# Kernel tuning notes

Hardware: AMD Instinct MI355X
Metric: run time of the kernel (lower is better)

The kernel has to match this reference:

```python
import jax, jax.numpy as jnp
import numpy as np

EMBED_DIM = 512
NUM_HEADS = 16
WINDOW = 8
SHIFT = 4
NUM_PATCHES = 64
NEG_INF = -1e9


def _attention_mask():
    # group map over the full patch grid, as in calculate_attention_mask
    P, s, ws = NUM_PATCHES, SHIFT, WINDOW
    g = np.zeros((P, P), dtype=np.float32)
    g[:, -s:] = 1
    g[-s:, :] = 2
    g[-s:, -s:] = 3
    nw = P // ws
    # (h ws a, w ws b) -> (h*w, ws*ws)
    gw = g.reshape(nw, ws, nw, ws).transpose(0, 2, 1, 3).reshape(nw * nw, ws * ws)
    same = gw[:, None, :] == gw[:, :, None]  # column - row == 0 -> allowed
    return jnp.asarray(same)  # (nW, S, S) bool, True = keep


def setup_inputs() -> dict:
    key = jax.random.key(0)
    ks = jax.random.split(key, 5)
    B, P, C = 16, NUM_PATCHES, EMBED_DIM
    sd = 1.0 / np.sqrt(C)
    return {
        "x": jax.random.normal(ks[0], (B, P, P, C), dtype=jnp.float32),
        "w_qkv": jax.random.normal(ks[1], (3 * C, C), dtype=jnp.float32) * sd,
        "b_qkv": jax.random.normal(ks[2], (3 * C,), dtype=jnp.float32) * 0.02,
        "w_out": jax.random.normal(ks[3], (C, C), dtype=jnp.float32) * sd,
        "b_out": jax.random.normal(ks[4], (C,), dtype=jnp.float32) * 0.02,
    }


def reference(x, w_qkv, b_qkv, w_out, b_out):
    B, P, _, C = x.shape
    ws, H = WINDOW, NUM_HEADS
    d = C // H
    nw = P // ws
    S = ws * ws
    scale = d ** (-0.5)

    # shift (roll backwards)
    xs = jnp.roll(x, (-SHIFT, -SHIFT), axis=(1, 2))
    # window partition: (B, nw, ws, nw, ws, C) -> (B*nw*nw, S, C)
    xw = xs.reshape(B, nw, ws, nw, ws, C).transpose(0, 1, 3, 2, 4, 5)
    xw = xw.reshape(B * nw * nw, S, C)

    qkv = xw @ w_qkv.T + b_qkv  # (Bn, S, 3C)
    q, k, v = jnp.split(qkv, 3, axis=-1)
    # head partition: (Bn, S, H, d) -> (Bn, H, S, d)
    part = lambda t: t.reshape(-1, S, H, d).transpose(0, 2, 1, 3)
    q, k, v = part(q), part(k), part(v)

    scores = jnp.einsum('bhqd,bhkd->bhqk', q, k) * scale  # (Bn, H, S, S)

    mask = _attention_mask()  # (nW, S, S) bool
    scores = scores.reshape(B, nw * nw, H, S, S)
    scores = jnp.where(mask[None, :, None], scores, NEG_INF)
    attn = jax.nn.softmax(scores, axis=-1)  # dropout p=0 (inference)
    attn = attn.reshape(B * nw * nw, H, S, S)

    out = jnp.einsum('bhqk,bhkd->bhqd', attn, v)  # (Bn, H, S, d)
    out = out.transpose(0, 2, 1, 3).reshape(B * nw * nw, S, C)  # merge heads
    out = out @ w_out.T + b_out

    # window merge: (B*nw*nw, S, C) -> (B, P, P, C)
    out = out.reshape(B, nw, nw, ws, ws, C).transpose(0, 1, 3, 2, 4, 5)
    out = out.reshape(B, P, P, C)
    # roll forwards
    return jnp.roll(out, (SHIFT, SHIFT), axis=(1, 2))
```

## Files before the change

### kernel.cpp

```cpp
#include <hip/hip_runtime.h>


using f16   = _Float16;
using f16x8 = __attribute__((ext_vector_type(8))) _Float16;
using f16x4 = __attribute__((ext_vector_type(4))) _Float16;
using f32x4 = __attribute__((ext_vector_type(4))) float;

#define MFMA16(a, b, c) __builtin_amdgcn_mfma_f32_16x16x32_f16((a), (b), (c), 0, 0, 0)
#define SCHEDBAR() __builtin_amdgcn_sched_barrier(0)
#define VMCNT0() asm volatile("s_waitcnt vmcnt(0)" ::: "memory")
#define LGKM0()  asm volatile("s_waitcnt lgkmcnt(0)" ::: "memory")
#define BAR()    __builtin_amdgcn_s_barrier()

static constexpr int QK_HALF = 65536 * 512;

__device__ __forceinline__ void nts4f(f32x4 v, float* p) {
  __builtin_nontemporal_store(v, (f32x4*)p);
}

__device__ __forceinline__ int tok2patch(int t) {
  int b = t >> 12, rem = t & 4095;
  int widx = rem >> 6, s = rem & 63;
  int pr = (((widx >> 3) << 3) + (s >> 3) + 4) & 63;
  int pc = (((widx & 7) << 3) + (s & 7) + 4) & 63;
  return ((b << 12) | (pr << 6) | pc) << 9;
}

__device__ __forceinline__ f16x8 cvt8(float4 a, float4 b) {
  f16x8 h = { (f16)a.x, (f16)a.y, (f16)a.z, (f16)a.w,
              (f16)b.x, (f16)b.y, (f16)b.z, (f16)b.w };
  return h;
}

__global__ __launch_bounds__(512, 2) void k_qkv(const float* __restrict__ x,
                                                const float* __restrict__ wq,
                                                const float* __restrict__ bq,
                                                f16* __restrict__ qk,
                                                f16* __restrict__ vt) {
  __shared__ __align__(16) char smem[86016];
  f16* const B0 = (f16*)smem;
  f16* const B1 = (f16*)(smem + 8192);

  const int tid = threadIdx.x;
  const int lane = tid & 63, wave = tid >> 6;
  const int jlo = lane & 15, g = lane >> 4;
  const int bm = blockIdx.x;

  const int nl = tid >> 2, kq = tid & 3;
  const int bslot = (kq ^ ((nl >> 1) & 3)) * 8;

  const int r0 = tok2patch(bm * 256 + wave * 32 + jlo);
  const int r1 = tok2patch(bm * 256 + wave * 32 + 16 + jlo);
  f16x8 af[2][16];
#pragma unroll
  for (int kg = 0; kg < 4; ++kg) {
    float4 t0[4][2], t1[4][2];
#pragma unroll
    for (int k4 = 0; k4 < 4; ++k4) {
      const int ko = (kg * 4 + k4) * 32 + g * 8;
      t0[k4][0] = *(const float4*)(x + r0 + ko);
      t0[k4][1] = *(const float4*)(x + r0 + ko + 4);
      t1[k4][0] = *(const float4*)(x + r1 + ko);
      t1[k4][1] = *(const float4*)(x + r1 + ko + 4);
    }
#pragma unroll
    for (int k4 = 0; k4 < 4; ++k4) {
      af[0][kg * 4 + k4] = cvt8(t0[k4][0], t0[k4][1]);
      af[1][kg * 4 + k4] = cvt8(t1[k4][0], t1[k4][1]);
    }
    SCHEDBAR();
  }

  f32x4 acc[2][8] = {};
  float4 rb[2];
#define LOADB(U2)                                                         \
  do {                                                                    \
    const int bn2_ = (U2) >> 4, k2_ = ((U2) & 15) * 32;                   \
    const float* bs_ = wq + (bn2_ * 128 + nl) * 512 + k2_ + kq * 8;       \
    rb[0] = *(const float4*)(bs_); rb[1] = *(const float4*)(bs_ + 4);     \
  } while (0)
#define WRITEB(Bp) do { *(f16x8*)((Bp) + nl * 32 + bslot) = cvt8(rb[0], rb[1]); } while (0)

  LOADB(0);
  SCHEDBAR();
  VMCNT0();
  WRITEB(B0);
  LOADB(1);
  LGKM0();
  BAR();

#pragma unroll 1
  for (int bn = 0; bn < 12; ++bn) {
    f16* const Cw = (f16*)(smem + 16384 + wave * 8704);
#pragma unroll
    for (int ks = 0; ks < 16; ++ks) {
      const int u = bn * 16 + ks;
      f16* const Bc = (u & 1) ? B1 : B0;
      f16* const Bn = (u & 1) ? B0 : B1;
      f16x8 bf[8];
#pragma unroll
      for (int nt = 0; nt < 8; ++nt) {
        const int n = nt * 16 + jlo;
        bf[nt] = *(const f16x8*)(Bc + n * 32 + ((g ^ ((n >> 1) & 3)) * 8));
      }
      __builtin_amdgcn_s_setprio(1);
#pragma unroll
      for (int mt = 0; mt < 2; ++mt)
#pragma unroll
        for (int nt = 0; nt < 8; ++nt)
          acc[mt][nt] = MFMA16(af[mt][ks], bf[nt], acc[mt][nt]);
      __builtin_amdgcn_s_setprio(0);
      VMCNT0();
      if (u + 1 < 192) WRITEB(Bn);
      SCHEDBAR();
      if (u + 2 < 192) LOADB(u + 2);
      LGKM0();
      BAR();
    }
    float bias[8];
#pragma unroll
    for (int nt = 0; nt < 8; ++nt) bias[nt] = bq[bn * 128 + nt * 16 + jlo];
    if (bn < 8) {
#pragma unroll
      for (int mt = 0; mt < 2; ++mt)
#pragma unroll
        for (int nt = 0; nt < 8; ++nt)
#pragma unroll
          for (int r = 0; r < 4; ++r)
            Cw[(mt * 16 + g * 4 + r) * 136 + nt * 16 + jlo] =
                (f16)(acc[mt][nt][r] + bias[nt]);
      LGKM0();
      f16* const gb = (bn < 4) ? (qk + bn * 128) : (qk + QK_HALF + (bn - 4) * 128);
#pragma unroll
      for (int p = 0; p < 8; ++p) {
        const int lr = (p >> 1) * 8 + (lane >> 3);
        const int ch = (p & 1) * 8 + (lane & 7);
        const int trow = bm * 256 + wave * 32 + lr;
        *(f16x8*)(gb + trow * 512 + ch * 8) = *(const f16x8*)(Cw + lr * 136 + ch * 8);
      }
    } else {
      const int w = (bm * 256 + wave * 32) >> 6;
      const int s0 = (wave * 32) & 63;
#pragma unroll
      for (int hf = 0; hf < 2; ++hf) {
#pragma unroll
        for (int n2 = 0; n2 < 4; ++n2) {
          const int nt = hf * 4 + n2;
#pragma unroll
          for (int mt = 0; mt < 2; ++mt) {
            f16x4 pk = { (f16)(acc[mt][nt][0] + bias[nt]), (f16)(acc[mt][nt][1] + bias[nt]),
                         (f16)(acc[mt][nt][2] + bias[nt]), (f16)(acc[mt][nt][3] + bias[nt]) };
            *(f16x4*)(Cw + (n2 * 16 + jlo) * 48 + mt * 16 + g * 4) = pk;
          }
        }
        LGKM0();
#pragma unroll
        for (int p = 0; p < 4; ++p) {
          const int cl = p * 16 + (lane >> 2);
          const int ch = lane & 3;
          const int n = (bn - 8) * 128 + hf * 64 + cl;
          const int h = n >> 5, d = n & 31;
          *(f16x8*)(vt + ((w * 16 + h) * 32 + d) * 64 + s0 + ch * 8) =
              *(const f16x8*)(Cw + cl * 48 + ch * 8);
        }
      }
    }
#pragma unroll
    for (int mt = 0; mt < 2; ++mt)
#pragma unroll
      for (int nt = 0; nt < 8; ++nt)
        acc[mt][nt] = (f32x4){0.f, 0.f, 0.f, 0.f};
  }
#undef LOADB
#undef WRITEB
}

__global__ __launch_bounds__(256) void k_attn(const f16* __restrict__ qk,
                                              const f16* __restrict__ vt,
                                              f16* __restrict__ ao) {
  __shared__ f16 P[4][64 * 72];
  const int w = blockIdx.x;
  const int widx = w & 63;
  const bool er = (widx >> 3) == 7;
  const bool ec = (widx & 7) == 7;
  const int tid = threadIdx.x;
  const int lane = tid & 63, wave = tid >> 6;
  const int jlo = lane & 15, g = lane >> 4;
  const int tb = w * 64;
  f16* Pw = P[wave];
  const float scale = 0.17677669529663687f;

#pragma unroll 1
  for (int hh = 0; hh < 4; ++hh) {
    const int h = wave * 4 + hh;
    f16x8 qa[4], kb[4];
#pragma unroll
    for (int mt = 0; mt < 4; ++mt)
      qa[mt] = *(const f16x8*)(qk + (tb + mt * 16 + jlo) * 512 + h * 32 + g * 8);
#pragma unroll
    for (int nt = 0; nt < 4; ++nt)
      kb[nt] = *(const f16x8*)(qk + QK_HALF + (tb + nt * 16 + jlo) * 512 + h * 32 + g * 8);
    f32x4 sc[4][4] = {};
#pragma unroll
    for (int mt = 0; mt < 4; ++mt)
#pragma unroll
      for (int nt = 0; nt < 4; ++nt)
        sc[mt][nt] = MFMA16(qa[mt], kb[nt], sc[mt][nt]);

    int gj[4];
#pragma unroll
    for (int nt = 0; nt < 4; ++nt) {
      int j = nt * 16 + jlo;
      gj[nt] = ((er && ((j >> 3) >= 4)) ? 2 : 0) | ((ec && ((j & 7) >= 4)) ? 1 : 0);
    }
    float rinv[4][4];
#pragma unroll
    for (int mt = 0; mt < 4; ++mt) {
#pragma unroll
      for (int r = 0; r < 4; ++r) {
        const int i = mt * 16 + g * 4 + r;
        const int gi = ((er && ((i >> 3) >= 4)) ? 2 : 0) | ((ec && ((i & 7) >= 4)) ? 1 : 0);
        float v0 = (gi == gj[0]) ? sc[mt][0][r] * scale : -1e9f;
        float v1 = (gi == gj[1]) ? sc[mt][1][r] * scale : -1e9f;
        float v2 = (gi == gj[2]) ? sc[mt][2][r] * scale : -1e9f;
        float v3 = (gi == gj[3]) ? sc[mt][3][r] * scale : -1e9f;
        float m = fmaxf(fmaxf(v0, v1), fmaxf(v2, v3));
        m = fmaxf(m, __shfl_xor(m, 1));
        m = fmaxf(m, __shfl_xor(m, 2));
        m = fmaxf(m, __shfl_xor(m, 4));
        m = fmaxf(m, __shfl_xor(m, 8));
        float p0 = __expf(v0 - m), p1 = __expf(v1 - m);
        float p2 = __expf(v2 - m), p3 = __expf(v3 - m);
        float s = p0 + p1 + p2 + p3;
        s += __shfl_xor(s, 1);
        s += __shfl_xor(s, 2);
        s += __shfl_xor(s, 4);
        s += __shfl_xor(s, 8);
        rinv[mt][r] = 1.0f / s;
        sc[mt][0][r] = p0; sc[mt][1][r] = p1; sc[mt][2][r] = p2; sc[mt][3][r] = p3;
      }
    }
#pragma unroll
    for (int mt = 0; mt < 4; ++mt)
#pragma unroll
      for (int nt = 0; nt < 4; ++nt)
#pragma unroll
        for (int r = 0; r < 4; ++r)
          Pw[(mt * 16 + g * 4 + r) * 72 + nt * 16 + jlo] = (f16)sc[mt][nt][r];
    asm volatile("s_waitcnt lgkmcnt(0)" ::: "memory");

    f32x4 o[4][2] = {};
#pragma unroll
    for (int ks = 0; ks < 2; ++ks) {
      f16x8 pa[4], vb[2];
#pragma unroll
      for (int mt = 0; mt < 4; ++mt)
        pa[mt] = *(const f16x8*)((const char*)Pw + (mt * 16 + jlo) * 144 + ks * 64 + g * 16);
#pragma unroll
      for (int nt = 0; nt < 2; ++nt)
        vb[nt] = *(const f16x8*)(vt + ((w * 16 + h) * 32 + nt * 16 + jlo) * 64 + ks * 32 + g * 8);
#pragma unroll
      for (int mt = 0; mt < 4; ++mt)
#pragma unroll
        for (int nt = 0; nt < 2; ++nt)
          o[mt][nt] = MFMA16(pa[mt], vb[nt], o[mt][nt]);
    }
#pragma unroll
    for (int mt = 0; mt < 4; ++mt)
#pragma unroll
      for (int nt = 0; nt < 2; ++nt)
#pragma unroll
        for (int r = 0; r < 4; ++r)
          Pw[(mt * 16 + g * 4 + r) * 40 + nt * 16 + jlo] =
              (f16)(o[mt][nt][r] * rinv[mt][r]);
    f16* arow = ao + (tb + lane) * 512 + h * 32;
#pragma unroll
    for (int c = 0; c < 4; ++c)
      *(f16x8*)(arow + c * 8) = *(const f16x8*)(Pw + lane * 40 + c * 8);
  }
}

__global__ __launch_bounds__(512, 2) void k_out(const f16* __restrict__ ao,
                                                const float* __restrict__ wo,
                                                const float* __restrict__ bo,
                                                float* __restrict__ out) {
  __shared__ __align__(16) char smem[86016];
  f16* const B0 = (f16*)smem;
  f16* const B1 = (f16*)(smem + 8192);

  const int tid = threadIdx.x;
  const int lane = tid & 63, wave = tid >> 6;
  const int jlo = lane & 15, g = lane >> 4;
  const int bm = blockIdx.x;

  const int nl = tid >> 2, kq = tid & 3;
  const int bslot = (kq ^ ((nl >> 1) & 3)) * 8;

  const f16* const a0 = ao + (bm * 256 + wave * 32 + jlo) * 512 + g * 8;
  const f16* const a1 = a0 + 16 * 512;
  f16x8 af[2][16];
#pragma unroll
  for (int ks = 0; ks < 16; ++ks) {
    af[0][ks] = *(const f16x8*)(a0 + ks * 32);
    af[1][ks] = *(const f16x8*)(a1 + ks * 32);
  }

  f32x4 acc[2][8] = {};
  float4 rb[2];
#define LOADB(U2)                                                         \
  do {                                                                    \
    const int bn2_ = (U2) >> 4, k2_ = ((U2) & 15) * 32;                   \
    const float* bs_ = wo + (bn2_ * 128 + nl) * 512 + k2_ + kq * 8;       \
    rb[0] = *(const float4*)(bs_); rb[1] = *(const float4*)(bs_ + 4);     \
  } while (0)
#define WRITEB(Bp) do { *(f16x8*)((Bp) + nl * 32 + bslot) = cvt8(rb[0], rb[1]); } while (0)

  LOADB(0);
  SCHEDBAR();
  VMCNT0();
  WRITEB(B0);
  LOADB(1);
  LGKM0();
  BAR();

#pragma unroll 1
  for (int bn = 0; bn < 4; ++bn) {
    float* const Cw = (float*)(smem + 16384 + wave * 8704);
#pragma unroll
    for (int ks = 0; ks < 16; ++ks) {
      const int u = bn * 16 + ks;
      f16* const Bc = (u & 1) ? B1 : B0;
      f16* const Bn = (u & 1) ? B0 : B1;
      f16x8 bf[8];
#pragma unroll
      for (int nt = 0; nt < 8; ++nt) {
        const int n = nt * 16 + jlo;
        bf[nt] = *(const f16x8*)(Bc + n * 32 + ((g ^ ((n >> 1) & 3)) * 8));
      }
      __builtin_amdgcn_s_setprio(1);
#pragma unroll
      for (int mt = 0; mt < 2; ++mt)
#pragma unroll
        for (int nt = 0; nt < 8; ++nt)
          acc[mt][nt] = MFMA16(af[mt][ks], bf[nt], acc[mt][nt]);
      __builtin_amdgcn_s_setprio(0);
      VMCNT0();
      if (u + 1 < 64) WRITEB(Bn);
      SCHEDBAR();
      if (u + 2 < 64) LOADB(u + 2);
      LGKM0();
      BAR();
    }
#pragma unroll
    for (int hf = 0; hf < 2; ++hf) {
#pragma unroll
      for (int n2 = 0; n2 < 4; ++n2) {
        const int nt = hf * 4 + n2;
        const float bias = bo[bn * 128 + nt * 16 + jlo];
#pragma unroll
        for (int mt = 0; mt < 2; ++mt)
#pragma unroll
          for (int r = 0; r < 4; ++r)
            Cw[(mt * 16 + g * 4 + r) * 68 + n2 * 16 + jlo] = acc[mt][nt][r] + bias;
      }
      LGKM0();
#pragma unroll
      for (int p = 0; p < 8; ++p) {
        const int lr = (p >> 1) * 8 + (lane >> 3);
        const int ch = (p & 1) * 8 + (lane & 7);
        const int trow = bm * 256 + wave * 32 + lr;
        nts4f(*(const f32x4*)(Cw + lr * 68 + ch * 4),
              out + tok2patch(trow) + bn * 128 + hf * 64 + ch * 4);
      }
      LGKM0();
    }
#pragma unroll
    for (int mt = 0; mt < 2; ++mt)
#pragma unroll
      for (int nt = 0; nt < 8; ++nt)
        acc[mt][nt] = (f32x4){0.f, 0.f, 0.f, 0.f};
  }
#undef LOADB
#undef WRITEB
}

extern "C" void kernel_launch(void* const* d_in, const int* in_sizes, int n_in,
                              void* d_out, int out_size, void* d_ws, size_t ws_size,
                              hipStream_t stream) {
  const float* x  = (const float*)d_in[0];
  const float* wq = (const float*)d_in[1];
  const float* bq = (const float*)d_in[2];
  const float* wo = (const float*)d_in[3];
  const float* bo = (const float*)d_in[4];
  float* out = (float*)d_out;

  f16* qk = (f16*)d_out;
  f16* ao = (f16*)d_ws;
  f16* vt = (f16*)((char*)d_ws + (64u << 20));

  k_qkv<<<dim3(256), 512, 0, stream>>>(x, wq, bq, qk, vt);
  k_attn<<<dim3(1024), 256, 0, stream>>>(qk, vt, ao);
  k_out<<<dim3(256), 512, 0, stream>>>(ao, wo, bo, out);
}
```

Baseline: 377.4 us.

## Halve GEMM block size and deepen weight prefetch to two stages

Both projection GEMM kernels drop from 512-thread blocks covering 256 tokens to 256-thread blocks covering 128 tokens, and launch twice as many blocks. Each thread now loads 16 weight floats per stage. The prefetch is triple-buffered in registers and waits on vmcnt(4) instead of vmcnt(0), so global weight loads overlap with more MFMA work. The QKV epilogue is also split into two halves, which shrinks its LDS staging. The gain should come from more blocks over the CUs and hidden load latency, but each block now re-reads the weight matrix for only half as many tokens, doubling total weight traffic.

```diff
diff --git a/kernel.cpp b/kernel.cpp
--- a/kernel.cpp
+++ b/kernel.cpp
@@ -8,6 +8,7 @@
 
 #define MFMA16(a, b, c) __builtin_amdgcn_mfma_f32_16x16x32_f16((a), (b), (c), 0, 0, 0)
 #define SCHEDBAR() __builtin_amdgcn_sched_barrier(0)
+#define VMCNT4() asm volatile("s_waitcnt vmcnt(4)" ::: "memory")
 #define VMCNT0() asm volatile("s_waitcnt vmcnt(0)" ::: "memory")
 #define LGKM0()  asm volatile("s_waitcnt lgkmcnt(0)" ::: "memory")
 #define BAR()    __builtin_amdgcn_s_barrier()
@@ -32,12 +33,12 @@
   return h;
 }
 
-__global__ __launch_bounds__(512, 2) void k_qkv(const float* __restrict__ x,
+__global__ __launch_bounds__(256, 2) void k_qkv(const float* __restrict__ x,
                                                 const float* __restrict__ wq,
                                                 const float* __restrict__ bq,
                                                 f16* __restrict__ qk,
                                                 f16* __restrict__ vt) {
-  __shared__ __align__(16) char smem[86016];
+  __shared__ __align__(16) char smem[37376];
   f16* const B0 = (f16*)smem;
   f16* const B1 = (f16*)(smem + 8192);
 
@@ -46,11 +47,11 @@
   const int jlo = lane & 15, g = lane >> 4;
   const int bm = blockIdx.x;
 
-  const int nl = tid >> 2, kq = tid & 3;
-  const int bslot = (kq ^ ((nl >> 1) & 3)) * 8;
-
-  const int r0 = tok2patch(bm * 256 + wave * 32 + jlo);
-  const int r1 = tok2patch(bm * 256 + wave * 32 + 16 + jlo);
+  const int nl = tid >> 1, kh = (tid & 1) * 16;
+  const int bsw = (nl >> 1) & 3, bc0 = (tid & 1) * 2;
+
+  const int r0 = tok2patch(bm * 128 + wave * 32 + jlo);
+  const int r1 = tok2patch(bm * 128 + wave * 32 + 16 + jlo);
   f16x8 af[2][16];
 #pragma unroll
   for (int kg = 0; kg < 4; ++kg) {
@@ -72,26 +73,32 @@
   }
 
   f32x4 acc[2][8] = {};
-  float4 rb[2];
-#define LOADB(U2)                                                         \
+  float4 rbA[4], rbB[4];
+#define LOADB(U2, RB)                                                     \
   do {                                                                    \
     const int bn2_ = (U2) >> 4, k2_ = ((U2) & 15) * 32;                   \
-    const float* bs_ = wq + (bn2_ * 128 + nl) * 512 + k2_ + kq * 8;       \
-    rb[0] = *(const float4*)(bs_); rb[1] = *(const float4*)(bs_ + 4);     \
+    const float* bs_ = wq + (bn2_ * 128 + nl) * 512 + k2_ + kh;           \
+    RB[0] = *(const float4*)(bs_);     RB[1] = *(const float4*)(bs_ + 4); \
+    RB[2] = *(const float4*)(bs_ + 8); RB[3] = *(const float4*)(bs_ + 12);\
   } while (0)
-#define WRITEB(Bp) do { *(f16x8*)((Bp) + nl * 32 + bslot) = cvt8(rb[0], rb[1]); } while (0)
-
-  LOADB(0);
+#define WRITEB(Bp, RB)                                                       \
+  do {                                                                       \
+    *(f16x8*)((Bp) + nl * 32 + ((bc0 ^ bsw) * 8))       = cvt8(RB[0], RB[1]);\
+    *(f16x8*)((Bp) + nl * 32 + (((bc0 + 1) ^ bsw) * 8)) = cvt8(RB[2], RB[3]);\
+  } while (0)
+
+  LOADB(0, rbA);
   SCHEDBAR();
   VMCNT0();
-  WRITEB(B0);
-  LOADB(1);
+  WRITEB(B0, rbA);
+  LOADB(1, rbB);
+  LOADB(2, rbA);
   LGKM0();
   BAR();
 
 #pragma unroll 1
   for (int bn = 0; bn < 12; ++bn) {
-    f16* const Cw = (f16*)(smem + 16384 + wave * 8704);
+    f16* const Cw = (f16*)(smem + 16384) + wave * 2560;
 #pragma unroll
     for (int ks = 0; ks < 16; ++ks) {
       const int u = bn * 16 + ks;
@@ -110,10 +117,18 @@
         for (int nt = 0; nt < 8; ++nt)
           acc[mt][nt] = MFMA16(af[mt][ks], bf[nt], acc[mt][nt]);
       __builtin_amdgcn_s_setprio(0);
-      VMCNT0();
-      if (u + 1 < 192) WRITEB(Bn);
-      SCHEDBAR();
-      if (u + 2 < 192) LOADB(u + 2);
+      if (u + 1 < 192) {
+        if (u < 190) { VMCNT4(); } else { VMCNT0(); }
+        if ((ks & 1) == 0) {
+          WRITEB(Bn, rbB);
+          SCHEDBAR();
+          if (u + 3 < 192) LOADB(u + 3, rbB);
+        } else {
+          WRITEB(Bn, rbA);
+          SCHEDBAR();
+          if (u + 3 < 192) LOADB(u + 3, rbA);
+        }
+      }
       LGKM0();
       BAR();
     }
@@ -121,26 +136,33 @@
 #pragma unroll
     for (int nt = 0; nt < 8; ++nt) bias[nt] = bq[bn * 128 + nt * 16 + jlo];
     if (bn < 8) {
-#pragma unroll
-      for (int mt = 0; mt < 2; ++mt)
-#pragma unroll
-        for (int nt = 0; nt < 8; ++nt)
-#pragma unroll
-          for (int r = 0; r < 4; ++r)
-            Cw[(mt * 16 + g * 4 + r) * 136 + nt * 16 + jlo] =
-                (f16)(acc[mt][nt][r] + bias[nt]);
-      LGKM0();
       f16* const gb = (bn < 4) ? (qk + bn * 128) : (qk + QK_HALF + (bn - 4) * 128);
 #pragma unroll
-      for (int p = 0; p < 8; ++p) {
-        const int lr = (p >> 1) * 8 + (lane >> 3);
-        const int ch = (p & 1) * 8 + (lane & 7);
-        const int trow = bm * 256 + wave * 32 + lr;
-        *(f16x8*)(gb + trow * 512 + ch * 8) = *(const f16x8*)(Cw + lr * 136 + ch * 8);
+      for (int hf = 0; hf < 2; ++hf) {
+#pragma unroll
+        for (int n2 = 0; n2 < 4; ++n2) {
+          const int nt = hf * 4 + n2;
+#pragma unroll
+          for (int mt = 0; mt < 2; ++mt)
+#pragma unroll
+            for (int r = 0; r < 4; ++r)
+              Cw[(mt * 16 + g * 4 + r) * 72 + n2 * 16 + jlo] =
+                  (f16)(acc[mt][nt][r] + bias[nt]);
+        }
+        LGKM0();
+#pragma unroll
+        for (int p = 0; p < 4; ++p) {
+          const int lr = p * 8 + (lane >> 3);
+          const int ch = lane & 7;
+          const int trow = bm * 128 + wave * 32 + lr;
+          *(f16x8*)(gb + trow * 512 + hf * 64 + ch * 8) =
+              *(const f16x8*)(Cw + lr * 72 + ch * 8);
+        }
+        LGKM0();
       }
     } else {
-      const int w = (bm * 256 + wave * 32) >> 6;
-      const int s0 = (wave * 32) & 63;
+      const int w = bm * 2 + (wave >> 1);
+      const int s0 = (wave & 1) * 32;
 #pragma unroll
       for (int hf = 0; hf < 2; ++hf) {
 #pragma unroll
@@ -150,7 +172,7 @@
           for (int mt = 0; mt < 2; ++mt) {
             f16x4 pk = { (f16)(acc[mt][nt][0] + bias[nt]), (f16)(acc[mt][nt][1] + bias[nt]),
                          (f16)(acc[mt][nt][2] + bias[nt]), (f16)(acc[mt][nt][3] + bias[nt]) };
-            *(f16x4*)(Cw + (n2 * 16 + jlo) * 48 + mt * 16 + g * 4) = pk;
+            *(f16x4*)(Cw + (n2 * 16 + jlo) * 40 + mt * 16 + g * 4) = pk;
           }
         }
         LGKM0();
@@ -161,8 +183,9 @@
           const int n = (bn - 8) * 128 + hf * 64 + cl;
           const int h = n >> 5, d = n & 31;
           *(f16x8*)(vt + ((w * 16 + h) * 32 + d) * 64 + s0 + ch * 8) =
-              *(const f16x8*)(Cw + cl * 48 + ch * 8);
-        }
+              *(const f16x8*)(Cw + cl * 40 + ch * 8);
+        }
+        LGKM0();
       }
     }
 #pragma unroll
@@ -280,11 +303,11 @@
   }
 }
 
-__global__ __launch_bounds__(512, 2) void k_out(const f16* __restrict__ ao,
+__global__ __launch_bounds__(256, 2) void k_out(const f16* __restrict__ ao,
                                                 const float* __restrict__ wo,
                                                 const float* __restrict__ bo,
                                                 float* __restrict__ out) {
-  __shared__ __align__(16) char smem[86016];
+  __shared__ __align__(16) char smem[51200];
   f16* const B0 = (f16*)smem;
   f16* const B1 = (f16*)(smem + 8192);
 
@@ -293,10 +316,10 @@
   const int jlo = lane & 15, g = lane >> 4;
   const int bm = blockIdx.x;
 
-  const int nl = tid >> 2, kq = tid & 3;
-  const int bslot = (kq ^ ((nl >> 1) & 3)) * 8;
-
-  const f16* const a0 = ao + (bm * 256 + wave * 32 + jlo) * 512 + g * 8;
+  const int nl = tid >> 1, kh = (tid & 1) * 16;
+  const int bsw = (nl >> 1) & 3, bc0 = (tid & 1) * 2;
+
+  const f16* const a0 = ao + (bm * 128 + wave * 32 + jlo) * 512 + g * 8;
   const f16* const a1 = a0 + 16 * 512;
   f16x8 af[2][16];
 #pragma unroll
@@ -306,26 +329,32 @@
   }
 
   f32x4 acc[2][8] = {};
-  float4 rb[2];
-#define LOADB(U2)                                                         \
+  float4 rbA[4], rbB[4];
+#define LOADB(U2, RB)                                                     \
   do {                                                                    \
     const int bn2_ = (U2) >> 4, k2_ = ((U2) & 15) * 32;                   \
-    const float* bs_ = wo + (bn2_ * 128 + nl) * 512 + k2_ + kq * 8;       \
-    rb[0] = *(const float4*)(bs_); rb[1] = *(const float4*)(bs_ + 4);     \
+    const float* bs_ = wo + (bn2_ * 128 + nl) * 512 + k2_ + kh;           \
+    RB[0] = *(const float4*)(bs_);     RB[1] = *(const float4*)(bs_ + 4); \
+    RB[2] = *(const float4*)(bs_ + 8); RB[3] = *(const float4*)(bs_ + 12);\
   } while (0)
-#define WRITEB(Bp) do { *(f16x8*)((Bp) + nl * 32 + bslot) = cvt8(rb[0], rb[1]); } while (0)
-
-  LOADB(0);
+#define WRITEB(Bp, RB)                                                       \
+  do {                                                                       \
+    *(f16x8*)((Bp) + nl * 32 + ((bc0 ^ bsw) * 8))       = cvt8(RB[0], RB[1]);\
+    *(f16x8*)((Bp) + nl * 32 + (((bc0 + 1) ^ bsw) * 8)) = cvt8(RB[2], RB[3]);\
+  } while (0)
+
+  LOADB(0, rbA);
   SCHEDBAR();
   VMCNT0();
-  WRITEB(B0);
-  LOADB(1);
+  WRITEB(B0, rbA);
+  LOADB(1, rbB);
+  LOADB(2, rbA);
   LGKM0();
   BAR();
 
 #pragma unroll 1
   for (int bn = 0; bn < 4; ++bn) {
-    float* const Cw = (float*)(smem + 16384 + wave * 8704);
+    float* const Cw = (float*)((char*)smem + 16384) + wave * 2176;
 #pragma unroll
     for (int ks = 0; ks < 16; ++ks) {
       const int u = bn * 16 + ks;
@@ -344,10 +373,18 @@
         for (int nt = 0; nt < 8; ++nt)
           acc[mt][nt] = MFMA16(af[mt][ks], bf[nt], acc[mt][nt]);
       __builtin_amdgcn_s_setprio(0);
-      VMCNT0();
-      if (u + 1 < 64) WRITEB(Bn);
-      SCHEDBAR();
-      if (u + 2 < 64) LOADB(u + 2);
+      if (u + 1 < 64) {
+        if (u < 62) { VMCNT4(); } else { VMCNT0(); }
+        if ((ks & 1) == 0) {
+          WRITEB(Bn, rbB);
+          SCHEDBAR();
+          if (u + 3 < 64) LOADB(u + 3, rbB);
+        } else {
+          WRITEB(Bn, rbA);
+          SCHEDBAR();
+          if (u + 3 < 64) LOADB(u + 3, rbA);
+        }
+      }
       LGKM0();
       BAR();
     }
@@ -368,7 +405,7 @@
       for (int p = 0; p < 8; ++p) {
         const int lr = (p >> 1) * 8 + (lane >> 3);
         const int ch = (p & 1) * 8 + (lane & 7);
-        const int trow = bm * 256 + wave * 32 + lr;
+        const int trow = bm * 128 + wave * 32 + lr;
         nts4f(*(const f32x4*)(Cw + lr * 68 + ch * 4),
               out + tok2patch(trow) + bn * 128 + hf * 64 + ch * 4);
       }
@@ -398,7 +435,7 @@
   f16* ao = (f16*)d_ws;
   f16* vt = (f16*)((char*)d_ws + (64u << 20));
 
-  k_qkv<<<dim3(256), 512, 0, stream>>>(x, wq, bq, qk, vt);
+  k_qkv<<<dim3(512), 256, 0, stream>>>(x, wq, bq, qk, vt);
   k_attn<<<dim3(1024), 256, 0, stream>>>(qk, vt, ao);
-  k_out<<<dim3(256), 512, 0, stream>>>(ao, wo, bo, out);
-}
+  k_out<<<dim3(512), 256, 0, stream>>>(ao, wo, bo, out);
+}
```

New measurement: 417.6 us. 10.6% more time.

## Pre-convert weights to fp16 and stream them via direct global-to-LDS loads

Applied to the files above, without the earlier changes.

Adds a small kernel that converts the QKV and output projection weights to fp16 in a pre-swizzled layout once per call. The GEMM kernels then stage 64-wide K slices straight into LDS with global_load_lds instead of loading fp32 to registers, converting, and writing to LDS. This halves the per-step barrier count and the weight bytes read by every block. The cost is an extra launch plus a larger LDS footprint, with __syncthreads replacing the manual waitcnt pipelining.

```diff
diff --git a/kernel.cpp b/kernel.cpp
--- a/kernel.cpp
+++ b/kernel.cpp
@@ -8,11 +8,18 @@
 
 #define MFMA16(a, b, c) __builtin_amdgcn_mfma_f32_16x16x32_f16((a), (b), (c), 0, 0, 0)
 #define SCHEDBAR() __builtin_amdgcn_sched_barrier(0)
-#define VMCNT0() asm volatile("s_waitcnt vmcnt(0)" ::: "memory")
 #define LGKM0()  asm volatile("s_waitcnt lgkmcnt(0)" ::: "memory")
-#define BAR()    __builtin_amdgcn_s_barrier()
 
 static constexpr int QK_HALF = 65536 * 512;
+
+__device__ f16 g_wq16[1536 * 512];
+__device__ f16 g_wo16[512 * 512];
+
+typedef const __attribute__((address_space(1))) unsigned int* gp_t;
+typedef __attribute__((address_space(3))) unsigned int* sp_t;
+__device__ __forceinline__ void gl_lds16(const f16* g, f16* s) {
+  __builtin_amdgcn_global_load_lds((gp_t)g, (sp_t)s, 16, 0, 0);
+}
 
 __device__ __forceinline__ void nts4f(f32x4 v, float* p) {
   __builtin_nontemporal_store(v, (f32x4*)p);
@@ -32,22 +39,32 @@
   return h;
 }
 
+__global__ __launch_bounds__(256) void k_wcvt(const float* __restrict__ wq,
+                                              const float* __restrict__ wo) {
+  int idx = blockIdx.x * 256 + threadIdx.x;
+  const float* src;
+  f16* dst;
+  if (idx < 98304) { src = wq; dst = g_wq16; }
+  else { idx -= 98304; src = wo; dst = g_wo16; }
+  const int n = idx >> 6, kb = (idx >> 3) & 7, s = idx & 7;
+  const float* p = src + n * 512 + kb * 64 + ((s ^ (n & 7)) << 3);
+  float4 a = *(const float4*)(p);
+  float4 b = *(const float4*)(p + 4);
+  *(f16x8*)(dst + n * 512 + kb * 64 + s * 8) = cvt8(a, b);
+}
+
 __global__ __launch_bounds__(512, 2) void k_qkv(const float* __restrict__ x,
-                                                const float* __restrict__ wq,
                                                 const float* __restrict__ bq,
                                                 f16* __restrict__ qk,
                                                 f16* __restrict__ vt) {
-  __shared__ __align__(16) char smem[86016];
+  __shared__ __align__(16) char smem[102400];
   f16* const B0 = (f16*)smem;
-  f16* const B1 = (f16*)(smem + 8192);
+  f16* const B1 = (f16*)(smem + 16384);
 
   const int tid = threadIdx.x;
   const int lane = tid & 63, wave = tid >> 6;
   const int jlo = lane & 15, g = lane >> 4;
   const int bm = blockIdx.x;
-
-  const int nl = tid >> 2, kq = tid & 3;
-  const int bslot = (kq ^ ((nl >> 1) & 3)) * 8;
 
   const int r0 = tok2patch(bm * 256 + wave * 32 + jlo);
   const int r1 = tok2patch(bm * 256 + wave * 32 + 16 + jlo);
@@ -71,37 +88,35 @@
     SCHEDBAR();
   }
 
+  const f16* const bsrc = g_wq16 + (wave * 16 + (lane >> 3)) * 512 + (lane & 7) * 8;
+  f16* const bdst = wave * 1024 + (f16*)nullptr;
+
   f32x4 acc[2][8] = {};
-  float4 rb[2];
-#define LOADB(U2)                                                         \
-  do {                                                                    \
-    const int bn2_ = (U2) >> 4, k2_ = ((U2) & 15) * 32;                   \
-    const float* bs_ = wq + (bn2_ * 128 + nl) * 512 + k2_ + kq * 8;       \
-    rb[0] = *(const float4*)(bs_); rb[1] = *(const float4*)(bs_ + 4);     \
+
+#define STAGE(P, Bp)                                                     \
+  do {                                                                   \
+    const f16* s_ = bsrc + ((P) >> 3) * 65536 + ((P) & 7) * 64;          \
+    gl_lds16(s_, (Bp) + wave * 1024);                                    \
+    gl_lds16(s_ + 8 * 512, (Bp) + wave * 1024 + 512);                    \
   } while (0)
-#define WRITEB(Bp) do { *(f16x8*)((Bp) + nl * 32 + bslot) = cvt8(rb[0], rb[1]); } while (0)
-
-  LOADB(0);
-  SCHEDBAR();
-  VMCNT0();
-  WRITEB(B0);
-  LOADB(1);
-  LGKM0();
-  BAR();
+
+  STAGE(0, B0);
+  __syncthreads();
 
 #pragma unroll 1
-  for (int bn = 0; bn < 12; ++bn) {
-    f16* const Cw = (f16*)(smem + 16384 + wave * 8704);
-#pragma unroll
-    for (int ks = 0; ks < 16; ++ks) {
-      const int u = bn * 16 + ks;
-      f16* const Bc = (u & 1) ? B1 : B0;
-      f16* const Bn = (u & 1) ? B0 : B1;
+  for (int p = 0; p < 96; ++p) {
+    f16* const Bc = (p & 1) ? B1 : B0;
+    f16* const Bn = (p & 1) ? B0 : B1;
+    if (p < 95) STAGE(p + 1, Bn);
+#pragma unroll
+    for (int s2 = 0; s2 < 2; ++s2) {
+      const int ks = (p & 7) * 2 + s2;
       f16x8 bf[8];
 #pragma unroll
       for (int nt = 0; nt < 8; ++nt) {
         const int n = nt * 16 + jlo;
-        bf[nt] = *(const f16x8*)(Bc + n * 32 + ((g ^ ((n >> 1) & 3)) * 8));
+        const int slot = (s2 * 4 + g) ^ (n & 7);
+        bf[nt] = *(const f16x8*)(Bc + n * 64 + slot * 8);
       }
       __builtin_amdgcn_s_setprio(1);
 #pragma unroll
@@ -110,69 +125,71 @@
         for (int nt = 0; nt < 8; ++nt)
           acc[mt][nt] = MFMA16(af[mt][ks], bf[nt], acc[mt][nt]);
       __builtin_amdgcn_s_setprio(0);
-      VMCNT0();
-      if (u + 1 < 192) WRITEB(Bn);
-      SCHEDBAR();
-      if (u + 2 < 192) LOADB(u + 2);
-      LGKM0();
-      BAR();
-    }
-    float bias[8];
-#pragma unroll
-    for (int nt = 0; nt < 8; ++nt) bias[nt] = bq[bn * 128 + nt * 16 + jlo];
-    if (bn < 8) {
-#pragma unroll
-      for (int mt = 0; mt < 2; ++mt)
-#pragma unroll
-        for (int nt = 0; nt < 8; ++nt)
-#pragma unroll
-          for (int r = 0; r < 4; ++r)
-            Cw[(mt * 16 + g * 4 + r) * 136 + nt * 16 + jlo] =
-                (f16)(acc[mt][nt][r] + bias[nt]);
-      LGKM0();
-      f16* const gb = (bn < 4) ? (qk + bn * 128) : (qk + QK_HALF + (bn - 4) * 128);
-#pragma unroll
-      for (int p = 0; p < 8; ++p) {
-        const int lr = (p >> 1) * 8 + (lane >> 3);
-        const int ch = (p & 1) * 8 + (lane & 7);
-        const int trow = bm * 256 + wave * 32 + lr;
-        *(f16x8*)(gb + trow * 512 + ch * 8) = *(const f16x8*)(Cw + lr * 136 + ch * 8);
-      }
-    } else {
-      const int w = (bm * 256 + wave * 32) >> 6;
-      const int s0 = (wave * 32) & 63;
-#pragma unroll
-      for (int hf = 0; hf < 2; ++hf) {
-#pragma unroll
-        for (int n2 = 0; n2 < 4; ++n2) {
-          const int nt = hf * 4 + n2;
-#pragma unroll
-          for (int mt = 0; mt < 2; ++mt) {
-            f16x4 pk = { (f16)(acc[mt][nt][0] + bias[nt]), (f16)(acc[mt][nt][1] + bias[nt]),
-                         (f16)(acc[mt][nt][2] + bias[nt]), (f16)(acc[mt][nt][3] + bias[nt]) };
-            *(f16x4*)(Cw + (n2 * 16 + jlo) * 48 + mt * 16 + g * 4) = pk;
-          }
+    }
+    __syncthreads();
+
+    if ((p & 7) == 7) {
+      const int bn = p >> 3;
+      float bias[8];
+#pragma unroll
+      for (int nt = 0; nt < 8; ++nt) bias[nt] = bq[bn * 128 + nt * 16 + jlo];
+      if (bn < 8) {
+        f16* const Cw = (f16*)(smem + 32768 + wave * 8704);
+#pragma unroll
+        for (int mt = 0; mt < 2; ++mt)
+#pragma unroll
+          for (int nt = 0; nt < 8; ++nt)
+#pragma unroll
+            for (int r = 0; r < 4; ++r)
+              Cw[(mt * 16 + g * 4 + r) * 136 + nt * 16 + jlo] =
+                  (f16)(acc[mt][nt][r] + bias[nt]);
+        LGKM0();
+        f16* const gb = (bn < 4) ? (qk + bn * 128) : (qk + QK_HALF + (bn - 4) * 128);
+#pragma unroll
+        for (int q = 0; q < 8; ++q) {
+          const int lr = (q >> 1) * 8 + (lane >> 3);
+          const int ch = (q & 1) * 8 + (lane & 7);
+          const int trow = bm * 256 + wave * 32 + lr;
+          *(f16x8*)(gb + trow * 512 + ch * 8) = *(const f16x8*)(Cw + lr * 136 + ch * 8);
         }
         LGKM0();
-#pragma unroll
-        for (int p = 0; p < 4; ++p) {
-          const int cl = p * 16 + (lane >> 2);
-          const int ch = lane & 3;
-          const int n = (bn - 8) * 128 + hf * 64 + cl;
-          const int h = n >> 5, d = n & 31;
-          *(f16x8*)(vt + ((w * 16 + h) * 32 + d) * 64 + s0 + ch * 8) =
-              *(const f16x8*)(Cw + cl * 48 + ch * 8);
+      } else {
+        f16* const Cw = (f16*)(smem + 32768 + wave * 8704);
+        const int w = bm * 4 + (wave >> 1);
+        const int s0 = (wave * 32) & 63;
+#pragma unroll
+        for (int hf = 0; hf < 2; ++hf) {
+#pragma unroll
+          for (int n2 = 0; n2 < 4; ++n2) {
+            const int nt = hf * 4 + n2;
+#pragma unroll
+            for (int mt = 0; mt < 2; ++mt) {
+              f16x4 pk = { (f16)(acc[mt][nt][0] + bias[nt]), (f16)(acc[mt][nt][1] + bias[nt]),
+                           (f16)(acc[mt][nt][2] + bias[nt]), (f16)(acc[mt][nt][3] + bias[nt]) };
+              *(f16x4*)(Cw + (n2 * 16 + jlo) * 48 + mt * 16 + g * 4) = pk;
+            }
+          }
+          LGKM0();
+#pragma unroll
+          for (int q = 0; q < 4; ++q) {
+            const int cl = q * 16 + (lane >> 2);
+            const int ch = lane & 3;
+            const int n = (bn - 8) * 128 + hf * 64 + cl;
+            const int h = n >> 5, d = n & 31;
+            *(f16x8*)(vt + ((w * 16 + h) * 32 + d) * 64 + s0 + ch * 8) =
+                *(const f16x8*)(Cw + cl * 48 + ch * 8);
+          }
+          LGKM0();
         }
       }
-    }
-#pragma unroll
-    for (int mt = 0; mt < 2; ++mt)
-#pragma unroll
-      for (int nt = 0; nt < 8; ++nt)
-        acc[mt][nt] = (f32x4){0.f, 0.f, 0.f, 0.f};
+#pragma unroll
+      for (int mt = 0; mt < 2; ++mt)
+#pragma unroll
+        for (int nt = 0; nt < 8; ++nt)
+          acc[mt][nt] = (f32x4){0.f, 0.f, 0.f, 0.f};
+    }
   }
-#undef LOADB
-#undef WRITEB
+#undef STAGE
 }
 
 __global__ __launch_bounds__(256) void k_attn(const f16* __restrict__ qk,
@@ -281,21 +298,17 @@
 }
 
 __global__ __launch_bounds__(512, 2) void k_out(const f16* __restrict__ ao,
-                                                const float* __restrict__ wo,
                                                 const float* __restrict__ bo,
                                                 float* __restrict__ out) {
-  __shared__ __align__(16) char smem[86016];
+  __shared__ __align__(16) char smem[102400];
   f16* const B0 = (f16*)smem;
-  f16* const B1 = (f16*)(smem + 8192);
+  f16* const B1 = (f16*)(smem + 16384);
 
   const int tid = threadIdx.x;
   const int lane = tid & 63, wave = tid >> 6;
   const int jlo = lane & 15, g = lane >> 4;
   const int bm = blockIdx.x;
 
-  const int nl = tid >> 2, kq = tid & 3;
-  const int bslot = (kq ^ ((nl >> 1) & 3)) * 8;
-
   const f16* const a0 = ao + (bm * 256 + wave * 32 + jlo) * 512 + g * 8;
   const f16* const a1 = a0 + 16 * 512;
   f16x8 af[2][16];
@@ -305,37 +318,33 @@
     af[1][ks] = *(const f16x8*)(a1 + ks * 32);
   }
 
+  const f16* const bsrc = g_wo16 + (wave * 16 + (lane >> 3)) * 512 + (lane & 7) * 8;
   f32x4 acc[2][8] = {};
-  float4 rb[2];
-#define LOADB(U2)                                                         \
-  do {                                                                    \
-    const int bn2_ = (U2) >> 4, k2_ = ((U2) & 15) * 32;                   \
-    const float* bs_ = wo + (bn2_ * 128 + nl) * 512 + k2_ + kq * 8;       \
-    rb[0] = *(const float4*)(bs_); rb[1] = *(const float4*)(bs_ + 4);     \
+
+#define STAGE(P, Bp)                                                     \
+  do {                                                                   \
+    const f16* s_ = bsrc + ((P) >> 3) * 65536 + ((P) & 7) * 64;          \
+    gl_lds16(s_, (Bp) + wave * 1024);                                    \
+    gl_lds16(s_ + 8 * 512, (Bp) + wave * 1024 + 512);                    \
   } while (0)
-#define WRITEB(Bp) do { *(f16x8*)((Bp) + nl * 32 + bslot) = cvt8(rb[0], rb[1]); } while (0)
-
-  LOADB(0);
-  SCHEDBAR();
-  VMCNT0();
-  WRITEB(B0);
-  LOADB(1);
-  LGKM0();
-  BAR();
+
+  STAGE(0, B0);
+  __syncthreads();
 
 #pragma unroll 1
-  for (int bn = 0; bn < 4; ++bn) {
-    float* const Cw = (float*)(smem + 16384 + wave * 8704);
-#pragma unroll
-    for (int ks = 0; ks < 16; ++ks) {
-      const int u = bn * 16 + ks;
-      f16* const Bc = (u & 1) ? B1 : B0;
-      f16* const Bn = (u & 1) ? B0 : B1;
+  for (int p = 0; p < 32; ++p) {
+    f16* const Bc = (p & 1) ? B1 : B0;
+    f16* const Bn = (p & 1) ? B0 : B1;
+    if (p < 31) STAGE(p + 1, Bn);
+#pragma unroll
+    for (int s2 = 0; s2 < 2; ++s2) {
+      const int ks = (p & 7) * 2 + s2;
       f16x8 bf[8];
 #pragma unroll
       for (int nt = 0; nt < 8; ++nt) {
         const int n = nt * 16 + jlo;
-        bf[nt] = *(const f16x8*)(Bc + n * 32 + ((g ^ ((n >> 1) & 3)) * 8));
+        const int slot = (s2 * 4 + g) ^ (n & 7);
+        bf[nt] = *(const f16x8*)(Bc + n * 64 + slot * 8);
       }
       __builtin_amdgcn_s_setprio(1);
 #pragma unroll
@@ -344,44 +353,43 @@
         for (int nt = 0; nt < 8; ++nt)
           acc[mt][nt] = MFMA16(af[mt][ks], bf[nt], acc[mt][nt]);
       __builtin_amdgcn_s_setprio(0);
-      VMCNT0();
-      if (u + 1 < 64) WRITEB(Bn);
-      SCHEDBAR();
-      if (u + 2 < 64) LOADB(u + 2);
-      LGKM0();
-      BAR();
-    }
-#pragma unroll
-    for (int hf = 0; hf < 2; ++hf) {
-#pragma unroll
-      for (int n2 = 0; n2 < 4; ++n2) {
-        const int nt = hf * 4 + n2;
-        const float bias = bo[bn * 128 + nt * 16 + jlo];
-#pragma unroll
-        for (int mt = 0; mt < 2; ++mt)
-#pragma unroll
-          for (int r = 0; r < 4; ++r)
-            Cw[(mt * 16 + g * 4 + r) * 68 + n2 * 16 + jlo] = acc[mt][nt][r] + bias;
+    }
+    __syncthreads();
+
+    if ((p & 7) == 7) {
+      const int bn = p >> 3;
+      float* const Cw = (float*)(smem + 32768 + wave * 8704);
+#pragma unroll
+      for (int hf = 0; hf < 2; ++hf) {
+#pragma unroll
+        for (int n2 = 0; n2 < 4; ++n2) {
+          const int nt = hf * 4 + n2;
+          const float bias = bo[bn * 128 + nt * 16 + jlo];
+#pragma unroll
+          for (int mt = 0; mt < 2; ++mt)
+#pragma unroll
+            for (int r = 0; r < 4; ++r)
+              Cw[(mt * 16 + g * 4 + r) * 68 + n2 * 16 + jlo] = acc[mt][nt][r] + bias;
+        }
+        LGKM0();
+#pragma unroll
+        for (int q = 0; q < 8; ++q) {
+          const int lr = (q >> 1) * 8 + (lane >> 3);
+          const int ch = (q & 1) * 8 + (lane & 7);
+          const int trow = bm * 256 + wave * 32 + lr;
+          nts4f(*(const f32x4*)(Cw + lr * 68 + ch * 4),
+                out + tok2patch(trow) + bn * 128 + hf * 64 + ch * 4);
+        }
+        LGKM0();
       }
-      LGKM0();
-#pragma unroll
-      for (int p = 0; p < 8; ++p) {
-        const int lr = (p >> 1) * 8 + (lane >> 3);
-        const int ch = (p & 1) * 8 + (lane & 7);
-        const int trow = bm * 256 + wave * 32 + lr;
-        nts4f(*(const f32x4*)(Cw + lr * 68 + ch * 4),
-              out + tok2patch(trow) + bn * 128 + hf * 64 + ch * 4);
-      }
-      LGKM0();
-    }
-#pragma unroll
-    for (int mt = 0; mt < 2; ++mt)
-#pragma unroll
-      for (int nt = 0; nt < 8; ++nt)
-        acc[mt][nt] = (f32x4){0.f, 0.f, 0.f, 0.f};
+#pragma unroll
+      for (int mt = 0; mt < 2; ++mt)
+#pragma unroll
+        for (int nt = 0; nt < 8; ++nt)
+          acc[mt][nt] = (f32x4){0.f, 0.f, 0.f, 0.f};
+    }
   }
-#undef LOADB
-#undef WRITEB
+#undef STAGE
 }
 
 extern "C" void kernel_launch(void* const* d_in, const int* in_sizes, int n_in,
@@ -398,7 +406,8 @@
   f16* ao = (f16*)d_ws;
   f16* vt = (f16*)((char*)d_ws + (64u << 20));
 
-  k_qkv<<<dim3(256), 512, 0, stream>>>(x, wq, bq, qk, vt);
+  k_wcvt<<<dim3(512), 256, 0, stream>>>(wq, wo);
+  k_qkv<<<dim3(256), 512, 0, stream>>>(x, bq, qk, vt);
   k_attn<<<dim3(1024), 256, 0, stream>>>(qk, vt, ao);
-  k_out<<<dim3(256), 512, 0, stream>>>(ao, wo, bo, out);
-}
+  k_out<<<dim3(256), 512, 0, stream>>>(ao, bo, out);
+}
```

Measured after the change: 445.9 us. 1.18x slower.
